# Performance work log

Measured on AMD Instinct MI355X. Metric: run time of the kernel, lower is better.

Reference implementation:

```python
import jax, jax.numpy as jnp
import numpy as np

M, K = 4096, 4096
ORDER = 12  # ceil(log2(max(M,K)))
BATCH, SEQ = 4, 2048


def _hilbert_d_grid(order, m, k):
    """Vectorized xy->d Hilbert-curve index for an m x k grid (numpy, int)."""
    n = 1 << order
    ii, jj = np.meshgrid(np.arange(m, dtype=np.int64), np.arange(k, dtype=np.int64), indexing='ij')
    x, y = jj.copy(), ii.copy()
    d = np.zeros_like(x)
    s = n >> 1
    while s > 0:
        rx = ((x & s) > 0).astype(np.int64)
        ry = ((y & s) > 0).astype(np.int64)
        d += s * s * ((3 * rx) ^ ry)
        # rotate quadrant
        swap = ry == 0
        flip = swap & (rx == 1)
        xf = np.where(flip, s - 1 - x, x)
        yf = np.where(flip, s - 1 - y, y)
        x = np.where(swap, yf, xf)
        y = np.where(swap, xf, yf)
        s >>= 1
    return d.astype(np.int32)


def setup_inputs() -> dict:
    key = jax.random.key(0)
    k1, = jax.random.split(key, 1)
    x = jax.random.normal(k1, (BATCH, SEQ, K), dtype=jnp.float32)
    # dna init per __init__: [4.0,1.0,1.0,0.5,0.5,0.5] with dna[0] += (seed%100)/10 for seed=42
    dna = jnp.array([8.2, 1.0, 1.0, 0.5, 0.5, 0.5], dtype=jnp.float32)
    bias = jnp.zeros((M,), dtype=jnp.float32)
    hilbert_d = jnp.asarray(_hilbert_d_grid(ORDER, M, K))  # [M, K] int32
    return {"x": x, "dna": dna, "bias": bias, "hilbert_d": hilbert_d}


def reference(x, dna, bias, hilbert_d):
    # dna is detached in the torch forward (weights built from numpy copy)
    p = jax.lax.stop_gradient(dna)
    m_p, a, b, n1, n2, n3 = p[0], p[1], p[2], p[3], p[4], p[5]
    total = jnp.float32((1 << ORDER) * (1 << ORDER))
    theta = hilbert_d.astype(jnp.float32) * (2.0 * jnp.pi / total)  # [M,K]
    ang = m_p * theta * 0.25
    base = jnp.abs(jnp.cos(ang) / a) ** n2 + jnp.abs(jnp.sin(ang) / b) ** n3
    r = base ** (-1.0 / n1)  # Gielis superformula radius, [M,K]
    w = (r - r.mean()) / (jnp.std(r, ddof=1) + 1e-9)  # torch .std() is unbiased
    scale = jnp.float32(1.0 / np.sqrt(K))
    return jnp.einsum('bsk,mk->bsm', x, w) * scale + bias
```

## Files before the change

kernel.cpp:

```cpp
#include <hip/hip_runtime.h>

#define M_DIM 4096
#define K_DIM 4096
#define NR_DIM 8192
#define TOTAL_ELEMS (M_DIM * K_DIM)

typedef unsigned short u16;
typedef unsigned int u32;
typedef __bf16 bf16x8 __attribute__((ext_vector_type(8)));
typedef float f32x4 __attribute__((ext_vector_type(4)));
typedef u16 u16x8 __attribute__((ext_vector_type(8)));

__device__ __forceinline__ u16 f2b(float f) {
    u32 v;
    __builtin_memcpy(&v, &f, sizeof(v));
    v += 0x7FFFu + ((v >> 16) & 1u);
    return (u16)(v >> 16);
}

__device__ __forceinline__ void abs_sincos(float ang, float* s, float* c) {
    float q = rintf(ang * 0.636619772f);
    float r1 = fmaf(q, -1.57079637e+00f, ang);
    float r = fmaf(q, 4.37113883e-08f, r1);
    float r2 = r * r;
    float ts = fmaf(r2, -1.9840874e-04f, 8.3333310e-03f);
    ts = fmaf(r2, ts, -1.6666667e-01f);
    float sp = fmaf(r * r2, ts, r);
    float tc = fmaf(r2, -1.3888378e-03f, 4.1666638e-02f);
    tc = fmaf(r2, tc, -5.0e-01f);
    float cp = fmaf(r2, tc, 1.0f);
    bool sw = (((int)q) & 1) != 0;
    *s = sw ? cp : sp;
    *c = sw ? sp : cp;
}

__device__ __forceinline__ float compute_r_fast(int d, float c_ang) {
    float s, c;
    abs_sincos((float)d * c_ang, &s, &c);
    float base = __builtin_amdgcn_sqrtf(fabsf(c)) + __builtin_amdgcn_sqrtf(fabsf(s));
    return __builtin_amdgcn_rcpf(base * base);
}

__device__ __noinline__ float compute_r_gen(int d, float c_ang, float inv_a,
                                            float inv_b, float n2, float n3, float e) {
    float s, c;
    abs_sincos((float)d * c_ang, &s, &c);
    float ca = fabsf(c) * fabsf(inv_a);
    float sb = fabsf(s) * fabsf(inv_b);
    float t1 = (n2 == 0.5f) ? sqrtf(ca) : ((n2 == 1.0f) ? ca : powf(ca, n2));
    float t2 = (n3 == 0.5f) ? sqrtf(sb) : ((n3 == 1.0f) ? sb : powf(sb, n3));
    float base = t1 + t2;
    if (e == -2.0f) { float ib = __builtin_amdgcn_rcpf(base); return ib * ib; }
    if (e == -1.0f) return __builtin_amdgcn_rcpf(base);
    return powf(base, e);
}

__device__ __forceinline__ bool dna_is_fast(const float* p) {
    return (p[1] == 1.0f) & (p[2] == 1.0f) & (p[3] == 0.5f) &
           (p[4] == 0.5f) & (p[5] == 0.5f);
}

__global__ void __launch_bounds__(256) reduce_kernel(const float* __restrict__ dna,
                                                     double* __restrict__ sums) {
    float p[6];
#pragma unroll
    for (int i = 0; i < 6; i++) p[i] = dna[i];
    float c_ang = (float)((double)p[0] * 6.283185307179586 / 67108864.0);

    double s = 0.0, s2 = 0.0;
    int idx = blockIdx.x * blockDim.x + threadIdx.x;
    int stride = gridDim.x * blockDim.x;
    if (dna_is_fast(p)) {
        for (int d = idx; d < TOTAL_ELEMS; d += stride) {
            float r = compute_r_fast(d, c_ang);
            s += (double)r;
            s2 += (double)r * (double)r;
        }
    } else {
        float inv_a = 1.0f / p[1], inv_b = 1.0f / p[2], e = -1.0f / p[3];
        for (int d = idx; d < TOTAL_ELEMS; d += stride) {
            float r = compute_r_gen(d, c_ang, inv_a, inv_b, p[4], p[5], e);
            s += (double)r;
            s2 += (double)r * (double)r;
        }
    }
#pragma unroll
    for (int off = 32; off > 0; off >>= 1) {
        s += __shfl_down(s, off);
        s2 += __shfl_down(s2, off);
    }
    __shared__ double ls[4], ls2[4];
    int lane = threadIdx.x & 63, w = threadIdx.x >> 6;
    if (lane == 0) { ls[w] = s; ls2[w] = s2; }
    __syncthreads();
    if (threadIdx.x == 0) {
        atomicAdd(&sums[0], ls[0] + ls[1] + ls[2] + ls[3]);
        atomicAdd(&sums[1], ls2[0] + ls2[1] + ls2[2] + ls2[3]);
    }
}

__global__ void __launch_bounds__(256) build_w_kernel(const int* __restrict__ hd,
                                                      const float* __restrict__ dna,
                                                      const double* __restrict__ sums,
                                                      u16* __restrict__ W) {
    float p[6];
#pragma unroll
    for (int i = 0; i < 6; i++) p[i] = dna[i];
    float c_ang = (float)((double)p[0] * 6.283185307179586 / 67108864.0);

    const double cnt = (double)TOTAL_ELEMS;
    double sum = sums[0], sumsq = sums[1];
    float meanf = (float)(sum / cnt);
    float stdf = (float)sqrt((sumsq - sum * sum / cnt) / (cnt - 1.0));
    float sc = 0.015625f / (stdf + 1e-9f);

    int idx = blockIdx.x * blockDim.x + threadIdx.x;
    int stride = gridDim.x * blockDim.x;
    if (dna_is_fast(p)) {
        for (int i = idx * 4; i < TOTAL_ELEMS; i += stride * 4) {
            int4 d4 = *(const int4*)(hd + i);
            ushort4 o;
            o.x = f2b((compute_r_fast(d4.x, c_ang) - meanf) * sc);
            o.y = f2b((compute_r_fast(d4.y, c_ang) - meanf) * sc);
            o.z = f2b((compute_r_fast(d4.z, c_ang) - meanf) * sc);
            o.w = f2b((compute_r_fast(d4.w, c_ang) - meanf) * sc);
            *(ushort4*)(W + i) = o;
        }
    } else {
        float inv_a = 1.0f / p[1], inv_b = 1.0f / p[2], e = -1.0f / p[3];
        for (int i = idx * 4; i < TOTAL_ELEMS; i += stride * 4) {
            int4 d4 = *(const int4*)(hd + i);
            ushort4 o;
            o.x = f2b((compute_r_gen(d4.x, c_ang, inv_a, inv_b, p[4], p[5], e) - meanf) * sc);
            o.y = f2b((compute_r_gen(d4.y, c_ang, inv_a, inv_b, p[4], p[5], e) - meanf) * sc);
            o.z = f2b((compute_r_gen(d4.z, c_ang, inv_a, inv_b, p[4], p[5], e) - meanf) * sc);
            o.w = f2b((compute_r_gen(d4.w, c_ang, inv_a, inv_b, p[4], p[5], e) - meanf) * sc);
            *(ushort4*)(W + i) = o;
        }
    }
}

__global__ void __launch_bounds__(256) convert_x_kernel(const float* __restrict__ x,
                                                        u16* __restrict__ xb) {
    int i = (blockIdx.x * blockDim.x + threadIdx.x) * 8;
    const float4* xv = (const float4*)(x + i);
    float4 a = xv[0], b = xv[1];
    u16x8 o;
    o[0] = f2b(a.x); o[1] = f2b(a.y); o[2] = f2b(a.z); o[3] = f2b(a.w);
    o[4] = f2b(b.x); o[5] = f2b(b.y); o[6] = f2b(b.z); o[7] = f2b(b.w);
    *(u16x8*)(xb + i) = o;
}

#define TM 128
#define TN 128
#define TK 64

__device__ __forceinline__ void gld_lds16(const u16* g, u16* l) {
    __builtin_amdgcn_global_load_lds(
        (const __attribute__((address_space(1))) void*)g,
        (__attribute__((address_space(3))) void*)l,
        16, 0, 0);
}

__global__ void __launch_bounds__(256) gemm_kernel(const u16* __restrict__ A,
                                                   const u16* __restrict__ B,
                                                   const float* __restrict__ bias,
                                                   float* __restrict__ C) {
    __shared__ __align__(16) u16 As[TM * TK];
    __shared__ __align__(16) u16 Bs[TN * TK];

    const int t = threadIdx.x;
    const int lane = t & 63;
    const int wave = t >> 6;
    const int wr = wave >> 1;
    const int wc = wave & 1;
    const int lrow = lane & 15;
    const int lq = lane >> 4;
    const int sw8 = lrow & 7;

    const long i0 = (long)blockIdx.y * TM;
    const long j0 = (long)blockIdx.x * TN;

    const int srow = t >> 3;
    const int scol = (((t & 7) ^ (srow & 7)) * 8);
    const int ldst = srow * TK + (t & 7) * 8;

    const f32x4 vzero = {0.f, 0.f, 0.f, 0.f};
    f32x4 acc[4][4];
#pragma unroll
    for (int a = 0; a < 4; a++)
#pragma unroll
        for (int b = 0; b < 4; b++) acc[a][b] = vzero;

    const u16* Ab = A + i0 * K_DIM;
    const u16* Bb = B + j0 * K_DIM;

    for (int k0 = 0; k0 < K_DIM; k0 += TK) {
#pragma unroll
        for (int q = 0; q < 4; q++) {
            int row = srow + q * 32;
            gld_lds16(Ab + (long)row * K_DIM + k0 + scol, &As[ldst + q * 32 * TK]);
        }
#pragma unroll
        for (int q = 0; q < 4; q++) {
            int row = srow + q * 32;
            gld_lds16(Bb + (long)row * K_DIM + k0 + scol, &Bs[ldst + q * 32 * TK]);
        }
        __syncthreads();

#pragma unroll
        for (int kk = 0; kk < TK; kk += 32) {
            const int kc = (kk >> 3) + lq;
            bf16x8 af[4], bfr[4];
#pragma unroll
            for (int mi = 0; mi < 4; mi++) {
                int row = wr * 64 + mi * 16 + lrow;
                af[mi] = *(const bf16x8*)(&As[row * TK + ((kc ^ sw8) << 3)]);
            }
#pragma unroll
            for (int ni = 0; ni < 4; ni++) {
                int row = wc * 64 + ni * 16 + lrow;
                bfr[ni] = *(const bf16x8*)(&Bs[row * TK + ((kc ^ sw8) << 3)]);
            }
#pragma unroll
            for (int mi = 0; mi < 4; mi++)
#pragma unroll
                for (int ni = 0; ni < 4; ni++)
                    acc[mi][ni] = __builtin_amdgcn_mfma_f32_16x16x32_bf16(
                        af[mi], bfr[ni], acc[mi][ni], 0, 0, 0);
        }
        __syncthreads();
    }

#pragma unroll
    for (int ni = 0; ni < 4; ni++) {
        long j = j0 + wc * 64 + ni * 16 + lrow;
        float bv = bias[j];
#pragma unroll
        for (int mi = 0; mi < 4; mi++) {
            long ib = i0 + wr * 64 + mi * 16 + lq * 4;
#pragma unroll
            for (int r = 0; r < 4; r++) {
                C[(ib + r) * M_DIM + j] = acc[mi][ni][r] + bv;
            }
        }
    }
}

extern "C" void kernel_launch(void* const* d_in, const int* in_sizes, int n_in,
                              void* d_out, int out_size, void* d_ws, size_t ws_size,
                              hipStream_t stream) {
    const float* x = (const float*)d_in[0];
    const float* dna = (const float*)d_in[1];
    const float* bias = (const float*)d_in[2];
    const int* hd = (const int*)d_in[3];
    float* out = (float*)d_out;

    double* sums = (double*)d_ws;
    u16* W = (u16*)((char*)d_ws + 256);
    u16* Xb = (u16*)((char*)d_ws + 256 + (size_t)TOTAL_ELEMS * 2);

    hipMemsetAsync(d_ws, 0, 256, stream);
    reduce_kernel<<<dim3(1024), dim3(256), 0, stream>>>(dna, sums);
    build_w_kernel<<<dim3(2048), dim3(256), 0, stream>>>(hd, dna, sums, W);
    convert_x_kernel<<<dim3((NR_DIM * K_DIM) / (256 * 8)), dim3(256), 0, stream>>>(x, Xb);
    gemm_kernel<<<dim3(M_DIM / TN, NR_DIM / TM), dim3(256), 0, stream>>>(Xb, W, bias, out);
}
```

Baseline: 601.9 us.

## Rewrite GEMM with 256x256 tiles, 8 waves, double-buffered LDS pipeline

Replaces the 128x128 single-buffered GEMM with a 256x256 block tile run by 512 threads (8 waves). The K loop is split into half-steps that prefetch the next K slices into double-buffered LDS while MFMAs run, with explicit vmcnt/lgkmcnt waits, barriers and setprio around MFMA groups. It also adds block-index swizzling for L2 locality and a new XOR LDS layout. The aim is to hide global-load latency and raise arithmetic intensity, at the cost of more registers, more LDS and fragile hand-placed waitcnt logic.

```diff
diff --git a/kernel.cpp b/kernel.cpp
--- a/kernel.cpp
+++ b/kernel.cpp
@@ -151,9 +151,9 @@
     *(u16x8*)(xb + i) = o;
 }
 
-#define TM 128
-#define TN 128
-#define TK 64
+#define BM 256
+#define BN 256
+#define BK 64
 
 __device__ __forceinline__ void gld_lds16(const u16* g, u16* l) {
     __builtin_amdgcn_global_load_lds(
@@ -162,85 +162,142 @@
         16, 0, 0);
 }
 
-__global__ void __launch_bounds__(256) gemm_kernel(const u16* __restrict__ A,
-                                                   const u16* __restrict__ B,
-                                                   const float* __restrict__ bias,
-                                                   float* __restrict__ C) {
-    __shared__ __align__(16) u16 As[TM * TK];
-    __shared__ __align__(16) u16 Bs[TN * TK];
-
-    const int t = threadIdx.x;
-    const int lane = t & 63;
-    const int wave = t >> 6;
-    const int wr = wave >> 1;
-    const int wc = wave & 1;
+#define FENCE asm volatile("" ::: "memory")
+#define WAIT_LGKM0 asm volatile("s_waitcnt lgkmcnt(0)" ::: "memory")
+#define WAIT_VM8 asm volatile("s_waitcnt vmcnt(8)" ::: "memory")
+
+#define LOAD_AF(h, bufv, ks)                                                  \
+    _Pragma("unroll") for (int m = 0; m < 4; ++m) {                           \
+        int row = wr * 128 + ((h) * 4 + m) * 16 + lrow;                       \
+        af[m] = *(const bf16x8*)(&sA[bufv][ks][row * 32 + oA]);               \
+    }
+
+#define LOAD_BF(bufv, ks)                                                     \
+    _Pragma("unroll") for (int n = 0; n < 4; ++n) {                           \
+        int row = wc * 64 + n * 16 + lrow;                                    \
+        bfr[n] = *(const bf16x8*)(&sB[bufv][ks][row * 32 + oA]);              \
+    }
+
+#define MFMA_HALF(h)                                                          \
+    __builtin_amdgcn_s_setprio(1);                                            \
+    _Pragma("unroll") for (int m = 0; m < 4; ++m)                             \
+        _Pragma("unroll") for (int n = 0; n < 4; ++n)                         \
+            acc[(h) * 4 + m][n] = __builtin_amdgcn_mfma_f32_16x16x32_bf16(    \
+                af[m], bfr[n], acc[(h) * 4 + m][n], 0, 0, 0);                 \
+    __builtin_amdgcn_s_setprio(0)
+
+__global__ void __launch_bounds__(512, 2) gemm_kernel(const u16* __restrict__ A,
+                                                      const u16* __restrict__ B,
+                                                      const float* __restrict__ bias,
+                                                      float* __restrict__ C) {
+    __shared__ __align__(16) u16 sA[2][2][BM * 32];
+    __shared__ __align__(16) u16 sB[2][2][BN * 32];
+
+    const int tid = threadIdx.x;
+    const int lane = tid & 63;
+    const int wave = tid >> 6;
+    const int wr = wave >> 2;
+    const int wc = wave & 3;
     const int lrow = lane & 15;
     const int lq = lane >> 4;
-    const int sw8 = lrow & 7;
-
-    const long i0 = (long)blockIdx.y * TM;
-    const long j0 = (long)blockIdx.x * TN;
-
-    const int srow = t >> 3;
-    const int scol = (((t & 7) ^ (srow & 7)) * 8);
-    const int ldst = srow * TK + (t & 7) * 8;
+    const int oA = ((lq ^ ((lrow >> 1) & 3)) << 3);
+
+    const int flat = blockIdx.y * 16 + blockIdx.x;
+    const int swz = (flat & 7) * 64 + (flat >> 3);
+    const int bx = swz & 15;
+    const int by = swz >> 4;
+    const int i0 = by * BM;
+    const int j0 = bx * BN;
+
+    const int srow0 = tid >> 2;
+    const int olog = (tid & 3) ^ ((srow0 >> 1) & 3);
+    const int aoff0 = (i0 + srow0) * K_DIM + olog * 8;
+    const int aoff1 = aoff0 + 128 * K_DIM;
+    const int boff0 = (j0 + srow0) * K_DIM + olog * 8;
+    const int boff1 = boff0 + 128 * K_DIM;
+    const int lds_l0 = tid * 8;
+    const int lds_l1 = (tid + 512) * 8;
+
+    auto stage = [&](const u16* base, int off0, int off1, u16* slot, int kb) {
+        gld_lds16(base + off0 + kb, slot + lds_l0);
+        gld_lds16(base + off1 + kb, slot + lds_l1);
+    };
 
     const f32x4 vzero = {0.f, 0.f, 0.f, 0.f};
-    f32x4 acc[4][4];
-#pragma unroll
-    for (int a = 0; a < 4; a++)
+    f32x4 acc[8][4];
+#pragma unroll
+    for (int a = 0; a < 8; a++)
 #pragma unroll
         for (int b = 0; b < 4; b++) acc[a][b] = vzero;
 
-    const u16* Ab = A + i0 * K_DIM;
-    const u16* Bb = B + j0 * K_DIM;
-
-    for (int k0 = 0; k0 < K_DIM; k0 += TK) {
-#pragma unroll
-        for (int q = 0; q < 4; q++) {
-            int row = srow + q * 32;
-            gld_lds16(Ab + (long)row * K_DIM + k0 + scol, &As[ldst + q * 32 * TK]);
-        }
-#pragma unroll
-        for (int q = 0; q < 4; q++) {
-            int row = srow + q * 32;
-            gld_lds16(Bb + (long)row * K_DIM + k0 + scol, &Bs[ldst + q * 32 * TK]);
-        }
-        __syncthreads();
-
-#pragma unroll
-        for (int kk = 0; kk < TK; kk += 32) {
-            const int kc = (kk >> 3) + lq;
-            bf16x8 af[4], bfr[4];
-#pragma unroll
-            for (int mi = 0; mi < 4; mi++) {
-                int row = wr * 64 + mi * 16 + lrow;
-                af[mi] = *(const bf16x8*)(&As[row * TK + ((kc ^ sw8) << 3)]);
-            }
-#pragma unroll
-            for (int ni = 0; ni < 4; ni++) {
-                int row = wc * 64 + ni * 16 + lrow;
-                bfr[ni] = *(const bf16x8*)(&Bs[row * TK + ((kc ^ sw8) << 3)]);
-            }
-#pragma unroll
-            for (int mi = 0; mi < 4; mi++)
-#pragma unroll
-                for (int ni = 0; ni < 4; ni++)
-                    acc[mi][ni] = __builtin_amdgcn_mfma_f32_16x16x32_bf16(
-                        af[mi], bfr[ni], acc[mi][ni], 0, 0, 0);
-        }
-        __syncthreads();
-    }
-
-#pragma unroll
-    for (int ni = 0; ni < 4; ni++) {
+    stage(A, aoff0, aoff1, sA[0][0], 0);
+    stage(B, boff0, boff1, sB[0][0], 0);
+    stage(A, aoff0, aoff1, sA[0][1], 32);
+    stage(B, boff0, boff1, sB[0][1], 32);
+    stage(A, aoff0, aoff1, sA[1][0], 64);
+    stage(B, boff0, boff1, sB[1][0], 64);
+    WAIT_VM8;
+    FENCE;
+    __builtin_amdgcn_s_barrier();
+
+    for (int kt = 0; kt < K_DIM / BK; ++kt) {
+        const int bufv = kt & 1;
+        const int kb1 = (kt + 1 < 64 ? kt + 1 : 63) * 64 + 32;
+        const int kb2 = (kt + 2 < 64 ? kt + 2 : 63) * 64;
+        bf16x8 af[4], bfr[4];
+
+        LOAD_AF(0, bufv, 0);
+        LOAD_BF(bufv, 0);
+        stage(A, aoff0, aoff1, sA[bufv ^ 1][1], kb1);
+        FENCE;
+        __builtin_amdgcn_s_barrier();
+        MFMA_HALF(0);
+        WAIT_LGKM0;
+        WAIT_VM8;
+        FENCE;
+        __builtin_amdgcn_s_barrier();
+
+        LOAD_AF(1, bufv, 0);
+        stage(B, boff0, boff1, sB[bufv ^ 1][1], kb1);
+        FENCE;
+        __builtin_amdgcn_s_barrier();
+        MFMA_HALF(1);
+        WAIT_LGKM0;
+        WAIT_VM8;
+        FENCE;
+        __builtin_amdgcn_s_barrier();
+
+        LOAD_AF(0, bufv, 1);
+        LOAD_BF(bufv, 1);
+        stage(A, aoff0, aoff1, sA[bufv][0], kb2);
+        FENCE;
+        __builtin_amdgcn_s_barrier();
+        MFMA_HALF(0);
+        WAIT_LGKM0;
+        WAIT_VM8;
+        FENCE;
+        __builtin_amdgcn_s_barrier();
+
+        LOAD_AF(1, bufv, 1);
+        stage(B, boff0, boff1, sB[bufv][0], kb2);
+        FENCE;
+        __builtin_amdgcn_s_barrier();
+        MFMA_HALF(1);
+        WAIT_LGKM0;
+        WAIT_VM8;
+        FENCE;
+        __builtin_amdgcn_s_barrier();
+    }
+
+#pragma unroll
+    for (int ni = 0; ni < 4; ++ni) {
         long j = j0 + wc * 64 + ni * 16 + lrow;
         float bv = bias[j];
 #pragma unroll
-        for (int mi = 0; mi < 4; mi++) {
-            long ib = i0 + wr * 64 + mi * 16 + lq * 4;
-#pragma unroll
-            for (int r = 0; r < 4; r++) {
+        for (int mi = 0; mi < 8; ++mi) {
+            long ib = i0 + wr * 128 + mi * 16 + lq * 4;
+#pragma unroll
+            for (int r = 0; r < 4; ++r) {
                 C[(ib + r) * M_DIM + j] = acc[mi][ni][r] + bv;
             }
         }
@@ -264,5 +321,5 @@
     reduce_kernel<<<dim3(1024), dim3(256), 0, stream>>>(dna, sums);
     build_w_kernel<<<dim3(2048), dim3(256), 0, stream>>>(hd, dna, sums, W);
     convert_x_kernel<<<dim3((NR_DIM * K_DIM) / (256 * 8)), dim3(256), 0, stream>>>(x, Xb);
-    gemm_kernel<<<dim3(M_DIM / TN, NR_DIM / TM), dim3(256), 0, stream>>>(Xb, W, bias, out);
-}
+    gemm_kernel<<<dim3(M_DIM / BN, NR_DIM / BM), dim3(512), 0, stream>>>(Xb, W, bias, out);
+}
```

After: 592.6 us. No clear change (-1.5%).
